# Kernel tuning notes

Measured on AMD Instinct MI355X. Metric: run time of the kernel, lower is better.

Reference implementation:

```python
import jax, jax.numpy as jnp
import numpy as np
from jax import lax

B, T, N, FIN = 1, 8, 50000, 3
E = 800000
HID, HEADS = 32, 2
NEG_SLOPE = 0.2  # PyG GATConv default negative_slope


def setup_inputs() -> dict:
    key = jax.random.key(0)
    ks = jax.random.split(key, 16)
    p = lambda k, shape: jax.random.normal(k, shape, dtype=jnp.float32) * 0.1
    return {
        "x_seq": jax.random.normal(ks[0], (B, T, N, FIN), dtype=jnp.float32),
        # GAT layer 1: lin weight [heads*hid, in], att vectors [heads, hid], bias [hid]
        "W1": p(ks[1], (HEADS * HID, FIN)),
        "a1_src": p(ks[2], (HEADS, HID)),
        "a1_dst": p(ks[3], (HEADS, HID)),
        "b1": p(ks[4], (HID,)),
        # GAT layer 2
        "W2": p(ks[5], (HEADS * HID, HID)),
        "a2_src": p(ks[6], (HEADS, HID)),
        "a2_dst": p(ks[7], (HEADS, HID)),
        "b2": p(ks[8], (HID,)),
        # GRU (single layer): torch layout [3*hid, hid] with gate order r,z,n
        "w_ih": p(ks[9], (3 * HID, HID)),
        "w_hh": p(ks[10], (3 * HID, HID)),
        "b_ih": p(ks[11], (3 * HID,)),
        "b_hh": p(ks[12], (3 * HID,)),
        # final Linear(hid, 1)
        "fc_w": p(ks[13], (1, HID)),
        "fc_b": p(ks[14], (1,)),
        "edge_index": jax.random.randint(ks[15], (2, E), 0, N, dtype=jnp.int64),
    }


def gat(x, src, dst, W, a_s, a_d, b):
    """PyG GATConv, heads=HEADS, concat=False (mean over heads). src/dst include self-loops."""
    n = x.shape[0]
    heads, hd = a_s.shape
    h = (x @ W.T).reshape(n, heads, hd)                      # [n, heads, hid]
    e = jax.nn.leaky_relu((h * a_s).sum(-1)[src] + (h * a_d).sum(-1)[dst], NEG_SLOPE)  # [E', heads]
    m = jax.ops.segment_max(e, dst, num_segments=n)          # per-destination max
    m = jnp.where(jnp.isfinite(m), m, jnp.zeros_like(m))
    ex = jnp.exp(e - m[dst])
    denom = jax.ops.segment_sum(ex, dst, num_segments=n)
    alpha = ex / (denom[dst] + 1e-16)                        # segment softmax
    out = jax.ops.segment_sum(h[src] * alpha[..., None], dst, num_segments=n)  # [n, heads, hid]
    return out.mean(axis=1) + b


def _forward(x_seq, W1, a1_src, a1_dst, b1, W2, a2_src, a2_dst, b2,
             w_ih, w_hh, b_ih, b_hh, fc_w, fc_b, edge_index):
    Bb, Tt, Nn, Fin = x_seq.shape
    n = Bb * Nn
    loops = jnp.arange(n, dtype=edge_index.dtype)            # add_self_loops=True
    src = jnp.concatenate([edge_index[0], loops])
    dst = jnp.concatenate([edge_index[1], loops])
    hid = b1.shape[0]

    def step(hstate, xt):                                    # one timestep: GAT x2 then GRU cell
        x = xt.reshape(n, Fin)
        g = jax.nn.relu(gat(x, src, dst, W1, a1_src, a1_dst, b1))
        g = jax.nn.relu(gat(g, src, dst, W2, a2_src, a2_dst, b2))
        gi = g @ w_ih.T + b_ih
        gh = hstate @ w_hh.T + b_hh
        i_r, i_z, i_n = jnp.split(gi, 3, axis=-1)
        h_r, h_z, h_n = jnp.split(gh, 3, axis=-1)
        r = jax.nn.sigmoid(i_r + h_r)
        z = jax.nn.sigmoid(i_z + h_z)
        cand = jnp.tanh(i_n + r * h_n)
        hnew = (1.0 - z) * cand + z * hstate
        return hnew, None

    h0 = jnp.zeros((n, hid), x_seq.dtype)
    h_final, _ = lax.scan(step, h0, jnp.moveaxis(x_seq, 1, 0))  # scan over T
    out = h_final @ fc_w.T + fc_b                            # [B*N, 1]
    return out.reshape(Bb, Nn)


def reference(x_seq, W1, a1_src, a1_dst, b1, W2, a2_src, a2_dst, b2,
              w_ih, w_hh, b_ih, b_hh, fc_w, fc_b, edge_index):
    return _forward(x_seq, W1, a1_src, a1_dst, b1, W2, a2_src, a2_dst, b2,
                    w_ih, w_hh, b_ih, b_hh, fc_w, fc_b, edge_index)
```

## Files before the change

kernel.cpp:

```cpp
#include <hip/hip_runtime.h>
#include <hip/hip_fp16.h>
#include <stdint.h>

#define T_STEPS 8
#define FIN 3
#define HID 32
#define NEG_SLOPE 0.2f
#define LOG2E 1.4426950408889634f

typedef __fp16 v4h __attribute__((ext_vector_type(4)));
typedef __fp16 v2h __attribute__((ext_vector_type(2)));
typedef float  v4f __attribute__((ext_vector_type(4)));

__device__ __forceinline__ float lrelu(float x) { return x > 0.f ? x : NEG_SLOPE * x; }
__device__ __forceinline__ float sigmoidf(float x) { return 1.f / (1.f + __expf(-x)); }

__device__ __forceinline__ float fdot2h(__half2 a, __half2 b, float c) {
#if __has_builtin(__builtin_amdgcn_fdot2)
    union { __half2 h; v2h v; } ua, ub;
    ua.h = a; ub.h = b;
    return __builtin_amdgcn_fdot2(ua.v, ub.v, c, false);
#else
    float2 fa = __half22float2(a), fb = __half22float2(b);
    return c + fa.x * fb.x + fa.y * fb.y;
#endif
}

__global__ void detect_kernel(const int* ei32, int nElems, int* flag) {
    __shared__ int any_nonzero;
    if (threadIdx.x == 0) any_nonzero = 0;
    __syncthreads();
    int idx = 1 + 2 * (int)threadIdx.x;
    if (idx < nElems && ei32[idx] != 0) any_nonzero = 1;
    __syncthreads();
    if (threadIdx.x == 0) *flag = (any_nonzero ? 0 : 1);
}

__device__ __forceinline__ int get_edge(const void* ei, int is64, long long idx) {
    if (is64) return (int)((const long long*)ei)[idx];
    return ((const int*)ei)[idx];
}

__global__ void init_kernel(int* cnt, int N) {
    int i = blockIdx.x * 256 + threadIdx.x;
    if (i < N) cnt[i] = 1;
}

__global__ void conv_count_kernel(const void* ei, const int* flag, int E, int N,
                                  int* src32, int* dst32, int* cnt) {
    int e = blockIdx.x * 256 + threadIdx.x;
    if (e >= E) return;
    int is64 = *flag;
    int s = get_edge(ei, is64, e);
    int d = get_edge(ei, is64, (long long)E + e);
    if ((unsigned)s >= (unsigned)N) s = 0;
    src32[e] = s;
    int dd = ((unsigned)d < (unsigned)N) ? d : 0x7fffffff;
    dst32[e] = dd;
    if (dd < N) atomicAdd(&cnt[dd], 1);
}

__global__ __launch_bounds__(256) void scan1_kernel(const int* cnt, int* rowptr, int* bsum, int n) {
    __shared__ int sm[256];
    int i = blockIdx.x * 256 + threadIdx.x;
    int v = (i < n) ? cnt[i] : 0;
    sm[threadIdx.x] = v;
    __syncthreads();
    for (int off = 1; off < 256; off <<= 1) {
        int t = (threadIdx.x >= off) ? sm[threadIdx.x - off] : 0;
        __syncthreads();
        sm[threadIdx.x] += t;
        __syncthreads();
    }
    if (i < n) rowptr[i + 1] = sm[threadIdx.x];
    if (threadIdx.x == 255) bsum[blockIdx.x] = sm[255];
}

__global__ __launch_bounds__(256) void scan2_kernel(int* bsum, int nb) {
    __shared__ int sm[256];
    int v = (threadIdx.x < nb) ? bsum[threadIdx.x] : 0;
    sm[threadIdx.x] = v;
    __syncthreads();
    for (int off = 1; off < 256; off <<= 1) {
        int t = (threadIdx.x >= off) ? sm[threadIdx.x - off] : 0;
        __syncthreads();
        sm[threadIdx.x] += t;
        __syncthreads();
    }
    if (threadIdx.x < nb) bsum[threadIdx.x] = sm[threadIdx.x];
}

__global__ __launch_bounds__(256) void scan3_kernel(int* rowptr, const int* bsum, int n) {
    int i = blockIdx.x * 256 + threadIdx.x;
    if (i < n && blockIdx.x > 0) rowptr[i + 1] += bsum[blockIdx.x - 1];
    if (i == 0) rowptr[0] = 0;
}

__global__ void selffill_kernel(const int* rowptr, int* csr, int* fill, int N) {
    int n = blockIdx.x * 256 + threadIdx.x;
    if (n >= N) return;
    int rp = rowptr[n];
    csr[rp] = n;
    fill[n] = rp + 1;
}

__global__ void scatter_kernel(const int* __restrict__ src32, const int* __restrict__ dst32,
                               int E, int lo, int hi, int* fill, int* csr) {
    int e = blockIdx.x * 256 + threadIdx.x;
    if (e >= E) return;
    int d = dst32[e];
    if (d < lo || d >= hi) return;
    int p = atomicAdd(&fill[d], 1);
    csr[p] = src32[e];
}

__global__ __launch_bounds__(64) void prep_u_kernel(
        const float* __restrict__ W2, const float* __restrict__ a2s,
        const float* __restrict__ a2d, float* __restrict__ u_s, float* __restrict__ u_d) {
    int l = threadIdx.x;
    int h = l >> 5, k = l & 31;
    float us = 0.f, ud = 0.f;
    for (int c = 0; c < 32; c++) {
        float w = W2[(h * 32 + c) * 32 + k];
        us += a2s[h * 32 + c] * w;
        ud += a2d[h * 32 + c] * w;
    }
    u_s[l] = us * LOG2E;
    u_d[l] = ud * LOG2E;
}

__global__ __launch_bounds__(256) void pack_kernel(
        const float* __restrict__ W2, __half2* __restrict__ w2h) {
    int idx = blockIdx.x * 256 + threadIdx.x;
    if (idx >= 1024) return;
    int kp = idx >> 6, r = idx & 63;
    float a = 0.5f * W2[r * 32 + 2 * kp];
    float b = 0.5f * W2[r * 32 + 2 * kp + 1];
    w2h[idx] = __floats2half2_rn(a, b);
}

__global__ __launch_bounds__(256) void packfrag_kernel(
        const float* __restrict__ w_ih, const float* __restrict__ w_hh,
        uint2* __restrict__ wfrag) {
    int idx = blockIdx.x * 256 + threadIdx.x;
    if (idx >= 1536) return;
    int q24 = idx >> 6, l = idx & 63;
    int c = l & 15, g = l >> 4;
    const float* W = (q24 < 12) ? w_ih : w_hh;
    int q = (q24 < 12) ? q24 : q24 - 12;
    int nt = q >> 1, kt = q & 1;
    float v[4];
#pragma unroll
    for (int b = 0; b < 4; b++) {
        int kk = kt * 16 + 4 * g + b;
        int nn = nt * 16 + c;
        v[b] = W[nn * 32 + kk];
    }
    __half2 lo = __floats2half2_rn(v[0], v[1]);
    __half2 hi = __floats2half2_rn(v[2], v[3]);
    uint2 u;
    u.x = *(unsigned*)&lo;
    u.y = *(unsigned*)&hi;
    wfrag[(8 + q24) * 64 + l] = u;
}

__global__ __launch_bounds__(256) void score1_all(
        const float* __restrict__ x_seq, const float* __restrict__ W1,
        const float* __restrict__ a1s, const float* __restrict__ a1d,
        float4* __restrict__ nrec4, float2* __restrict__ sd1, int N) {
    int t = blockIdx.x;
    int node = blockIdx.y * 256 + threadIdx.x;
    if (node >= N) return;
    const float* xp = x_seq + ((size_t)t * N + node) * FIN;
    float x0 = xp[0], x1 = xp[1], x2 = xp[2];
    float ps0 = 0.f, ps1 = 0.f, pd0 = 0.f, pd1 = 0.f;
    for (int c = 0; c < 32; c++) {
        float h0 = W1[c * 3] * x0 + W1[c * 3 + 1] * x1 + W1[c * 3 + 2] * x2;
        float h1 = W1[96 + c * 3] * x0 + W1[97 + c * 3] * x1 + W1[98 + c * 3] * x2;
        ps0 += h0 * a1s[c]; pd0 += h0 * a1d[c];
        ps1 += h1 * a1s[32 + c]; pd1 += h1 * a1d[32 + c];
    }
    ps0 *= LOG2E; ps1 *= LOG2E; pd0 *= LOG2E; pd1 *= LOG2E;
    unsigned u = (unsigned)__half_as_ushort(__float2half_rn(ps0)) |
                 ((unsigned)__half_as_ushort(__float2half_rn(ps1)) << 16);
    float4 r;
    r.x = x0; r.y = x1; r.z = x2; r.w = __uint_as_float(u);
    nrec4[(size_t)t * N + node] = r;
    sd1[(size_t)t * N + node] = make_float2(pd0, pd1);
}

__device__ __forceinline__ void unpack_scores(float wslot, float& s0, float& s1) {
    unsigned u = __float_as_uint(wslot);
    s0 = __half2float(__ushort_as_half((unsigned short)(u & 0xffffu)));
    s1 = __half2float(__ushort_as_half((unsigned short)(u >> 16)));
}

__global__ __launch_bounds__(64) void aggA_all(
        const int* __restrict__ rowptr, const int* __restrict__ csr,
        const float4* __restrict__ nrec4, const float2* __restrict__ sd1,
        const float* __restrict__ W1, const float* __restrict__ b1,
        const float* __restrict__ u_s, const float* __restrict__ u_d,
        __half2* __restrict__ g1h, float2* __restrict__ ssd2, float2* __restrict__ sd2, int N) {
    int t = blockIdx.x;
    int dst = blockIdx.y * 64 + threadIdx.x;
    if (dst >= N) return;
    const float4* nr = nrec4 + (size_t)t * N;
    int rs = rowptr[dst], re = rowptr[dst + 1];
    float2 sdv = sd1[(size_t)t * N + dst];
    float q0 = 0, qx0 = 0, qx1 = 0, qx2 = 0;
    float q1 = 0, qy0 = 0, qy1 = 0, qy2 = 0;
#define AGGA_EDGE(rr) { \
        float s0h, s1h; unpack_scores(rr.w, s0h, s1h); \
        float w0 = exp2f(lrelu(s0h + sdv.x)); \
        float w1 = exp2f(lrelu(s1h + sdv.y)); \
        q0 += w0; qx0 += w0 * rr.x; qx1 += w0 * rr.y; qx2 += w0 * rr.z; \
        q1 += w1; qy0 += w1 * rr.x; qy1 += w1 * rr.y; qy2 += w1 * rr.z; }
    int e = rs;
    for (; e + 4 <= re; e += 4) {
        int s0 = csr[e], s1 = csr[e + 1], s2 = csr[e + 2], s3 = csr[e + 3];
        float4 r0 = nr[s0], r1 = nr[s1], r2 = nr[s2], r3 = nr[s3];
        AGGA_EDGE(r0); AGGA_EDGE(r1); AGGA_EDGE(r2); AGGA_EDGE(r3);
    }
    for (; e < re; e++) {
        float4 r = nr[csr[e]];
        AGGA_EDGE(r);
    }
#undef AGGA_EDGE
    float inv0 = 1.f / (q0 + 1e-16f), inv1 = 1.f / (q1 + 1e-16f);
    float ax0 = qx0 * inv0, ax1 = qx1 * inv0, ax2 = qx2 * inv0;
    float ay0 = qy0 * inv1, ay1 = qy1 * inv1, ay2 = qy2 * inv1;
    float ps0 = 0, ps1 = 0, pd0 = 0, pd1 = 0;
    float4 out[4];
    __half2* ghp = (__half2*)out;
    float gprev = 0.f;
#pragma unroll
    for (int c = 0; c < 32; c++) {
        float v0 = W1[c * 3] * ax0 + W1[c * 3 + 1] * ax1 + W1[c * 3 + 2] * ax2;
        float v1 = W1[96 + c * 3] * ay0 + W1[97 + c * 3] * ay1 + W1[98 + c * 3] * ay2;
        float g = fmaxf(0.5f * (v0 + v1) + b1[c], 0.f);
        ps0 += g * u_s[c];      ps1 += g * u_s[32 + c];
        pd0 += g * u_d[c];      pd1 += g * u_d[32 + c];
        if (c & 1) ghp[c >> 1] = __floats2half2_rn(gprev, g);
        else gprev = g;
    }
    float4* gdst = (float4*)(g1h + (size_t)t * N * 16 + (size_t)dst * 16);
    gdst[0] = out[0]; gdst[1] = out[1]; gdst[2] = out[2]; gdst[3] = out[3];
    ssd2[(size_t)t * N + dst] = make_float2(ps0, ps1);
    sd2[(size_t)t * N + dst]  = make_float2(pd0, pd1);
}

__global__ __launch_bounds__(256) void aggBg2_all(
        const int* __restrict__ rowptr, const int* __restrict__ csr,
        const __half2* __restrict__ g1h,
        const float2* __restrict__ ssd2, const float2* __restrict__ sd2,
        const __half2* __restrict__ w2h, const float* __restrict__ b2,
        __half2* __restrict__ g2H, int N) {
    __shared__ __half2 a_lds[64 * 33];
    int t = blockIdx.x;
    int tid = threadIdx.x;
    int node0 = blockIdx.y * 64;
    int dl = tid >> 2;
    int q = tid & 3;
    int dst = node0 + dl;
    if (dst < N) {
        const __half2* gbase = g1h + (size_t)t * N * 16 + q * 4;
        const float2* ss = ssd2 + (size_t)t * N;
        int rs = rowptr[dst], re = rowptr[dst + 1];
        float2 sdv = sd2[(size_t)t * N + dst];
        float a0[8] = {0, 0, 0, 0, 0, 0, 0, 0};
        float a1[8] = {0, 0, 0, 0, 0, 0, 0, 0};
        float den0 = 0.f, den1 = 0.f;
#define AGGB_EDGE(sc, gv) { \
        float w0 = exp2f(lrelu(sc.x + sdv.x)); \
        float w1 = exp2f(lrelu(sc.y + sdv.y)); \
        den0 += w0; den1 += w1; \
        __half2 w0h = __float2half2_rn(w0); \
        __half2 w1h = __float2half2_rn(w1); \
        const __half2* p = (const __half2*)&(gv); \
        h0[0] = __hfma2(w0h, p[0], h0[0]); h0[1] = __hfma2(w0h, p[1], h0[1]); \
        h0[2] = __hfma2(w0h, p[2], h0[2]); h0[3] = __hfma2(w0h, p[3], h0[3]); \
        h1[0] = __hfma2(w1h, p[0], h1[0]); h1[1] = __hfma2(w1h, p[1], h1[1]); \
        h1[2] = __hfma2(w1h, p[2], h1[2]); h1[3] = __hfma2(w1h, p[3], h1[3]); }
        int e = rs;
        while (e < re) {
            int lim = min(re, e + 16);
            __half2 h0[4], h1[4];
#pragma unroll
            for (int j = 0; j < 4; j++) {
                h0[j] = __floats2half2_rn(0.f, 0.f);
                h1[j] = __floats2half2_rn(0.f, 0.f);
            }
            for (; e + 4 <= lim; e += 4) {
                int s0 = csr[e], s1 = csr[e + 1], s2 = csr[e + 2], s3 = csr[e + 3];
                float2 c0 = ss[s0], c1 = ss[s1], c2 = ss[s2], c3 = ss[s3];
                float4 g0 = *(const float4*)(gbase + (size_t)s0 * 16);
                float4 g1 = *(const float4*)(gbase + (size_t)s1 * 16);
                float4 g2 = *(const float4*)(gbase + (size_t)s2 * 16);
                float4 g3 = *(const float4*)(gbase + (size_t)s3 * 16);
                AGGB_EDGE(c0, g0); AGGB_EDGE(c1, g1); AGGB_EDGE(c2, g2); AGGB_EDGE(c3, g3);
            }
            for (; e < lim; e++) {
                int s = csr[e];
                float2 c = ss[s];
                float4 g = *(const float4*)(gbase + (size_t)s * 16);
                AGGB_EDGE(c, g);
            }
#pragma unroll
            for (int j = 0; j < 4; j++) {
                float2 v0 = __half22float2(h0[j]);
                float2 v1 = __half22float2(h1[j]);
                a0[2 * j] += v0.x; a0[2 * j + 1] += v0.y;
                a1[2 * j] += v1.x; a1[2 * j + 1] += v1.y;
            }
        }
#undef AGGB_EDGE
        float i0 = 1.f / (den0 + 1e-16f), i1 = 1.f / (den1 + 1e-16f);
#pragma unroll
        for (int j = 0; j < 4; j++) {
            a_lds[dl * 33 + q * 4 + j]      = __floats2half2_rn(a0[2 * j] * i0, a0[2 * j + 1] * i0);
            a_lds[dl * 33 + 16 + q * 4 + j] = __floats2half2_rn(a1[2 * j] * i1, a1[2 * j + 1] * i1);
        }
    }
    __syncthreads();
    int nl = tid & 63;
    int cg8 = __builtin_amdgcn_readfirstlane((tid >> 6) * 8);
    int node = node0 + nl;
    if (node >= N) return;
    float acc[8] = {0, 0, 0, 0, 0, 0, 0, 0};
    for (int kp = 0; kp < 16; kp++) {
        __half2 A0 = a_lds[nl * 33 + kp];
        __half2 A1 = a_lds[nl * 33 + 16 + kp];
        const __half2* w0p = w2h + kp * 64 + cg8;
        const __half2* w1p = w2h + kp * 64 + 32 + cg8;
#pragma unroll
        for (int j = 0; j < 8; j++) {
            acc[j] = fdot2h(A0, w0p[j], acc[j]);
            acc[j] = fdot2h(A1, w1p[j], acc[j]);
        }
    }
    __half2 o[4];
#pragma unroll
    for (int j = 0; j < 4; j++) {
        float ga = fmaxf(acc[2 * j] + b2[cg8 + 2 * j], 0.f);
        float gb = fmaxf(acc[2 * j + 1] + b2[cg8 + 2 * j + 1], 0.f);
        o[j] = __floats2half2_rn(ga, gb);
    }
    *(float4*)(g2H + ((size_t)t * N + node) * 16 + (cg8 >> 1)) = *(float4*)o;
}

__global__ __launch_bounds__(64) void gru_mfma(
        const __half2* __restrict__ g2H, const uint2* __restrict__ wfrag,
        const float* __restrict__ b_ih, const float* __restrict__ b_hh,
        const float* __restrict__ fc_w, const float* __restrict__ fc_b,
        float* __restrict__ out, int N) {
    __shared__ __align__(16) __half h_lds[16 * 36];
    int l = threadIdx.x;
    int c = l & 15;
    int g4 = l >> 4;
    int node0 = blockIdx.x * 16;
    union FU { uint2 u; v4h h; };
    v4h Bih[6][2], Bhh[6][2];
#pragma unroll
    for (int nt = 0; nt < 6; nt++)
#pragma unroll
        for (int kt = 0; kt < 2; kt++) {
            FU f; f.u = wfrag[(8 + nt * 2 + kt) * 64 + l]; Bih[nt][kt] = f.h;
            f.u = wfrag[(20 + nt * 2 + kt) * 64 + l]; Bhh[nt][kt] = f.h;
        }
    float bir0 = b_ih[c], bir1 = b_ih[c + 16];
    float biz0 = b_ih[32 + c], biz1 = b_ih[48 + c];
    float bin0 = b_ih[64 + c], bin1 = b_ih[80 + c];
    float bhr0 = b_hh[c], bhr1 = b_hh[c + 16];
    float bhz0 = b_hh[32 + c], bhz1 = b_hh[48 + c];
    float bhn0 = b_hh[64 + c], bhn1 = b_hh[80 + c];
    float fcw0 = fc_w[c], fcw1 = fc_w[c + 16];
    v4f hold0 = {0.f, 0.f, 0.f, 0.f};
    v4f hold1 = {0.f, 0.f, 0.f, 0.f};
    const __half2* rowb = g2H + (size_t)(node0 + c) * 16;
    for (int t = 0; t < T_STEPS; t++) {
        const __half2* rb = rowb + (size_t)t * N * 16;
        v4f Di[6], Dh[6];
#pragma unroll
        for (int nt = 0; nt < 6; nt++) { Di[nt] = {0.f, 0.f, 0.f, 0.f}; Dh[nt] = {0.f, 0.f, 0.f, 0.f}; }
#pragma unroll
        for (int kt = 0; kt < 2; kt++) {
            FU Ag; Ag.u = *(const uint2*)(rb + 2 * g4 + 8 * kt);
#pragma unroll
            for (int nt = 0; nt < 6; nt++)
                Di[nt] = __builtin_amdgcn_mfma_f32_16x16x16f16(Ag.h, Bih[nt][kt], Di[nt], 0, 0, 0);
        }
        if (t > 0) {
#pragma unroll
            for (int kt = 0; kt < 2; kt++) {
                FU Ah; Ah.u = *(const uint2*)&h_lds[c * 36 + 4 * g4 + 16 * kt];
#pragma unroll
                for (int nt = 0; nt < 6; nt++)
                    Dh[nt] = __builtin_amdgcn_mfma_f32_16x16x16f16(Ah.h, Bhh[nt][kt], Dh[nt], 0, 0, 0);
            }
        }
        v4f hn0, hn1;
#pragma unroll
        for (int i = 0; i < 4; i++) {
            {
                float rr = sigmoidf((Di[0][i] + bir0) + (Dh[0][i] + bhr0));
                float zz = sigmoidf((Di[2][i] + biz0) + (Dh[2][i] + bhz0));
                float cand = tanhf((Di[4][i] + bin0) + rr * (Dh[4][i] + bhn0));
                hn0[i] = (1.f - zz) * cand + zz * hold0[i];
            }
            {
                float rr = sigmoidf((Di[1][i] + bir1) + (Dh[1][i] + bhr1));
                float zz = sigmoidf((Di[3][i] + biz1) + (Dh[3][i] + bhz1));
                float cand = tanhf((Di[5][i] + bin1) + rr * (Dh[5][i] + bhn1));
                hn1[i] = (1.f - zz) * cand + zz * hold1[i];
            }
        }
        hold0 = hn0; hold1 = hn1;
        if (t < T_STEPS - 1) {
            __syncthreads();
#pragma unroll
            for (int i = 0; i < 4; i++) {
                int nrow = 4 * g4 + i;
                h_lds[nrow * 36 + c]      = __float2half_rn(hn0[i]);
                h_lds[nrow * 36 + c + 16] = __float2half_rn(hn1[i]);
            }
            __syncthreads();
        }
    }
#pragma unroll
    for (int i = 0; i < 4; i++) {
        float p = fcw0 * hold0[i] + fcw1 * hold1[i];
        p += __shfl_xor(p, 1, 64);
        p += __shfl_xor(p, 2, 64);
        p += __shfl_xor(p, 4, 64);
        p += __shfl_xor(p, 8, 64);
        if (c == 0) out[node0 + 4 * g4 + i] = p + fc_b[0];
    }
}

extern "C" void kernel_launch(void* const* d_in, const int* in_sizes, int n_in,
                              void* d_out, int out_size, void* d_ws, size_t ws_size,
                              hipStream_t stream) {
    const float* x_seq = (const float*)d_in[0];
    const float* W1  = (const float*)d_in[1];
    const float* a1s = (const float*)d_in[2];
    const float* a1d = (const float*)d_in[3];
    const float* b1  = (const float*)d_in[4];
    const float* W2  = (const float*)d_in[5];
    const float* a2s = (const float*)d_in[6];
    const float* a2d = (const float*)d_in[7];
    const float* b2  = (const float*)d_in[8];
    const float* w_ih = (const float*)d_in[9];
    const float* w_hh = (const float*)d_in[10];
    const float* b_ih = (const float*)d_in[11];
    const float* b_hh = (const float*)d_in[12];
    const float* fc_w = (const float*)d_in[13];
    const float* fc_b = (const float*)d_in[14];
    const void*  ei   = d_in[15];

    const int N = in_sizes[0] / (T_STEPS * FIN);
    const int E = in_sizes[15] / 2;
    const int NE = E + N;
    const int NB = (N + 255) / 256;
    const int NB64 = (N + 63) / 64;
    const int NB16 = (N + 15) / 16;
    const int EB = (E + 255) / 256;

    char* ws = (char*)d_ws;
    size_t off = 0;
    auto alloc = [&](size_t bytes) -> void* {
        void* p = ws + off;
        off += (bytes + 255) & ~(size_t)255;
        return p;
    };
    int*     flag   = (int*)alloc(4);
    int*     rowptr = (int*)alloc((size_t)(N + 1) * 4);
    int*     cnt    = (int*)alloc((size_t)N * 4);
    int*     bsum   = (int*)alloc(256 * 4);
    int*     csr    = (int*)alloc((size_t)NE * 4);
    int*     src32  = (int*)alloc((size_t)E * 4);
    int*     dst32  = (int*)alloc((size_t)E * 4);
    float4*  nrec4  = (float4*)alloc((size_t)T_STEPS * N * 16);
    float2*  sd1    = (float2*)alloc((size_t)T_STEPS * N * 8);
    float2*  ssd2   = (float2*)alloc((size_t)T_STEPS * N * 8);
    float2*  sd2    = (float2*)alloc((size_t)T_STEPS * N * 8);
    __half2* g1h    = (__half2*)alloc((size_t)T_STEPS * N * 16 * 4);
    __half2* g2H    = (__half2*)alloc((size_t)T_STEPS * N * 16 * 4);
    float*   u_s    = (float*)alloc(64 * 4);
    float*   u_d    = (float*)alloc(64 * 4);
    __half2* w2h    = (__half2*)alloc(1024 * 4);
    uint2*   wfrag  = (uint2*)alloc(32 * 64 * 8);
    if (off > ws_size) return;

    detect_kernel<<<1, 128, 0, stream>>>((const int*)ei, in_sizes[15], flag);
    init_kernel<<<NB, 256, 0, stream>>>(cnt, N);
    conv_count_kernel<<<EB, 256, 0, stream>>>(ei, flag, E, N, src32, dst32, cnt);
    scan1_kernel<<<NB, 256, 0, stream>>>(cnt, rowptr, bsum, N);
    scan2_kernel<<<1, 256, 0, stream>>>(bsum, NB);
    scan3_kernel<<<NB, 256, 0, stream>>>(rowptr, bsum, N);
    selffill_kernel<<<NB, 256, 0, stream>>>(rowptr, csr, cnt, N);
    {
        const int NPASS = 2;
        int per = (N + NPASS - 1) / NPASS;
        for (int p = 0; p < NPASS; p++) {
            int lo = p * per;
            int hi = min(lo + per, N);
            scatter_kernel<<<EB, 256, 0, stream>>>(src32, dst32, E, lo, hi, cnt, csr);
        }
    }
    prep_u_kernel<<<1, 64, 0, stream>>>(W2, a2s, a2d, u_s, u_d);
    pack_kernel<<<4, 256, 0, stream>>>(W2, w2h);
    packfrag_kernel<<<6, 256, 0, stream>>>(w_ih, w_hh, wfrag);

    score1_all<<<dim3(T_STEPS, NB), 256, 0, stream>>>(x_seq, W1, a1s, a1d, nrec4, sd1, N);
    aggA_all<<<dim3(T_STEPS, NB64), 64, 0, stream>>>(rowptr, csr, nrec4, sd1, W1, b1,
                                                     u_s, u_d, g1h, ssd2, sd2, N);
    aggBg2_all<<<dim3(T_STEPS, NB64), 256, 0, stream>>>(rowptr, csr, g1h, ssd2, sd2,
                                                        w2h, b2, g2H, N);
    gru_mfma<<<NB16, 64, 0, stream>>>(g2H, wfrag, b_ih, b_hh,
                                      fc_w, fc_b, (float*)d_out, N);
}
```

Before: 289.8 us.

## Process one destination node per thread in layer-2 aggregation and projection

The layer-2 aggregation kernel drops the four-threads-per-node split with an LDS staging buffer and a block barrier. Each thread now owns one destination node. It gathers full 64-byte source rows, accumulates all 32 channels for both heads, and does the full 32x32 projection in registers before writing its output row. This removes the LDS round trip, the synchronization and the redundant per-node score/rowptr loads. In exchange it sharply raises register pressure (64 float accumulators plus 32 half2 partials), lowers gather parallelism per node and increases divergence across nodes of different degree.

```diff
diff --git a/kernel.cpp b/kernel.cpp
--- a/kernel.cpp
+++ b/kernel.cpp
@@ -255,97 +255,91 @@
         const float2* __restrict__ ssd2, const float2* __restrict__ sd2,
         const __half2* __restrict__ w2h, const float* __restrict__ b2,
         __half2* __restrict__ g2H, int N) {
-    __shared__ __half2 a_lds[64 * 33];
     int t = blockIdx.x;
-    int tid = threadIdx.x;
-    int node0 = blockIdx.y * 64;
-    int dl = tid >> 2;
-    int q = tid & 3;
-    int dst = node0 + dl;
-    if (dst < N) {
-        const __half2* gbase = g1h + (size_t)t * N * 16 + q * 4;
-        const float2* ss = ssd2 + (size_t)t * N;
-        int rs = rowptr[dst], re = rowptr[dst + 1];
-        float2 sdv = sd2[(size_t)t * N + dst];
-        float a0[8] = {0, 0, 0, 0, 0, 0, 0, 0};
-        float a1[8] = {0, 0, 0, 0, 0, 0, 0, 0};
-        float den0 = 0.f, den1 = 0.f;
-#define AGGB_EDGE(sc, gv) { \
+    int dst = blockIdx.y * 256 + threadIdx.x;
+    if (dst >= N) return;
+    const __half2* gt = g1h + (size_t)t * N * 16;
+    const float2* ss = ssd2 + (size_t)t * N;
+    int rs = rowptr[dst], re = rowptr[dst + 1];
+    float2 sdv = sd2[(size_t)t * N + dst];
+    float den0 = 0.f, den1 = 0.f;
+    float a0f[32], a1f[32];
+#pragma unroll
+    for (int j = 0; j < 32; j++) { a0f[j] = 0.f; a1f[j] = 0.f; }
+    union Row { float4 f[4]; __half2 h[16]; };
+#define AGGB_EDGE(sc, rr) { \
         float w0 = exp2f(lrelu(sc.x + sdv.x)); \
         float w1 = exp2f(lrelu(sc.y + sdv.y)); \
         den0 += w0; den1 += w1; \
         __half2 w0h = __float2half2_rn(w0); \
         __half2 w1h = __float2half2_rn(w1); \
-        const __half2* p = (const __half2*)&(gv); \
-        h0[0] = __hfma2(w0h, p[0], h0[0]); h0[1] = __hfma2(w0h, p[1], h0[1]); \
-        h0[2] = __hfma2(w0h, p[2], h0[2]); h0[3] = __hfma2(w0h, p[3], h0[3]); \
-        h1[0] = __hfma2(w1h, p[0], h1[0]); h1[1] = __hfma2(w1h, p[1], h1[1]); \
-        h1[2] = __hfma2(w1h, p[2], h1[2]); h1[3] = __hfma2(w1h, p[3], h1[3]); }
-        int e = rs;
-        while (e < re) {
-            int lim = min(re, e + 16);
-            __half2 h0[4], h1[4];
-#pragma unroll
-            for (int j = 0; j < 4; j++) {
-                h0[j] = __floats2half2_rn(0.f, 0.f);
-                h1[j] = __floats2half2_rn(0.f, 0.f);
-            }
-            for (; e + 4 <= lim; e += 4) {
-                int s0 = csr[e], s1 = csr[e + 1], s2 = csr[e + 2], s3 = csr[e + 3];
-                float2 c0 = ss[s0], c1 = ss[s1], c2 = ss[s2], c3 = ss[s3];
-                float4 g0 = *(const float4*)(gbase + (size_t)s0 * 16);
-                float4 g1 = *(const float4*)(gbase + (size_t)s1 * 16);
-                float4 g2 = *(const float4*)(gbase + (size_t)s2 * 16);
-                float4 g3 = *(const float4*)(gbase + (size_t)s3 * 16);
-                AGGB_EDGE(c0, g0); AGGB_EDGE(c1, g1); AGGB_EDGE(c2, g2); AGGB_EDGE(c3, g3);
-            }
-            for (; e < lim; e++) {
-                int s = csr[e];
-                float2 c = ss[s];
-                float4 g = *(const float4*)(gbase + (size_t)s * 16);
-                AGGB_EDGE(c, g);
-            }
-#pragma unroll
-            for (int j = 0; j < 4; j++) {
-                float2 v0 = __half22float2(h0[j]);
-                float2 v1 = __half22float2(h1[j]);
-                a0[2 * j] += v0.x; a0[2 * j + 1] += v0.y;
-                a1[2 * j] += v1.x; a1[2 * j + 1] += v1.y;
-            }
-        }
+        _Pragma("unroll") \
+        for (int j = 0; j < 16; j++) { \
+            p0[j] = __hfma2(w0h, rr.h[j], p0[j]); \
+            p1[j] = __hfma2(w1h, rr.h[j], p1[j]); \
+        } }
+    int e = rs;
+    while (e < re) {
+        int lim = min(re, e + 16);
+        __half2 p0[16], p1[16];
+        __half2 z = __floats2half2_rn(0.f, 0.f);
+#pragma unroll
+        for (int j = 0; j < 16; j++) { p0[j] = z; p1[j] = z; }
+        for (; e + 2 <= lim; e += 2) {
+            int s0 = csr[e], s1 = csr[e + 1];
+            float2 c0 = ss[s0], c1 = ss[s1];
+            const float4* r0p = (const float4*)(gt + (size_t)s0 * 16);
+            const float4* r1p = (const float4*)(gt + (size_t)s1 * 16);
+            Row r0, r1;
+            r0.f[0] = r0p[0]; r0.f[1] = r0p[1]; r0.f[2] = r0p[2]; r0.f[3] = r0p[3];
+            r1.f[0] = r1p[0]; r1.f[1] = r1p[1]; r1.f[2] = r1p[2]; r1.f[3] = r1p[3];
+            AGGB_EDGE(c0, r0);
+            AGGB_EDGE(c1, r1);
+        }
+        for (; e < lim; e++) {
+            int s = csr[e];
+            float2 c = ss[s];
+            const float4* rp = (const float4*)(gt + (size_t)s * 16);
+            Row r;
+            r.f[0] = rp[0]; r.f[1] = rp[1]; r.f[2] = rp[2]; r.f[3] = rp[3];
+            AGGB_EDGE(c, r);
+        }
+#pragma unroll
+        for (int j = 0; j < 16; j++) {
+            float2 v0 = __half22float2(p0[j]);
+            float2 v1 = __half22float2(p1[j]);
+            a0f[2 * j] += v0.x; a0f[2 * j + 1] += v0.y;
+            a1f[2 * j] += v1.x; a1f[2 * j + 1] += v1.y;
+        }
+    }
 #undef AGGB_EDGE
-        float i0 = 1.f / (den0 + 1e-16f), i1 = 1.f / (den1 + 1e-16f);
-#pragma unroll
-        for (int j = 0; j < 4; j++) {
-            a_lds[dl * 33 + q * 4 + j]      = __floats2half2_rn(a0[2 * j] * i0, a0[2 * j + 1] * i0);
-            a_lds[dl * 33 + 16 + q * 4 + j] = __floats2half2_rn(a1[2 * j] * i1, a1[2 * j + 1] * i1);
-        }
-    }
-    __syncthreads();
-    int nl = tid & 63;
-    int cg8 = __builtin_amdgcn_readfirstlane((tid >> 6) * 8);
-    int node = node0 + nl;
-    if (node >= N) return;
-    float acc[8] = {0, 0, 0, 0, 0, 0, 0, 0};
-    for (int kp = 0; kp < 16; kp++) {
-        __half2 A0 = a_lds[nl * 33 + kp];
-        __half2 A1 = a_lds[nl * 33 + 16 + kp];
-        const __half2* w0p = w2h + kp * 64 + cg8;
-        const __half2* w1p = w2h + kp * 64 + 32 + cg8;
-#pragma unroll
-        for (int j = 0; j < 8; j++) {
-            acc[j] = fdot2h(A0, w0p[j], acc[j]);
-            acc[j] = fdot2h(A1, w1p[j], acc[j]);
-        }
-    }
-    __half2 o[4];
-#pragma unroll
-    for (int j = 0; j < 4; j++) {
-        float ga = fmaxf(acc[2 * j] + b2[cg8 + 2 * j], 0.f);
-        float gb = fmaxf(acc[2 * j + 1] + b2[cg8 + 2 * j + 1], 0.f);
-        o[j] = __floats2half2_rn(ga, gb);
-    }
-    *(float4*)(g2H + ((size_t)t * N + node) * 16 + (cg8 >> 1)) = *(float4*)o;
+    float i0 = 1.f / (den0 + 1e-16f), i1 = 1.f / (den1 + 1e-16f);
+    __half2 an0[16], an1[16];
+#pragma unroll
+    for (int j = 0; j < 16; j++) {
+        an0[j] = __floats2half2_rn(a0f[2 * j] * i0, a0f[2 * j + 1] * i0);
+        an1[j] = __floats2half2_rn(a1f[2 * j] * i1, a1f[2 * j + 1] * i1);
+    }
+    __half2 og[16];
+#pragma unroll
+    for (int cp = 0; cp < 16; cp++) {
+        float accA = 0.f, accB = 0.f;
+#pragma unroll
+        for (int kp = 0; kp < 16; kp++) {
+            accA = fdot2h(an0[kp], w2h[kp * 64 + 2 * cp], accA);
+            accA = fdot2h(an1[kp], w2h[kp * 64 + 32 + 2 * cp], accA);
+            accB = fdot2h(an0[kp], w2h[kp * 64 + 2 * cp + 1], accB);
+            accB = fdot2h(an1[kp], w2h[kp * 64 + 32 + 2 * cp + 1], accB);
+        }
+        float ga = fmaxf(accA + b2[2 * cp], 0.f);
+        float gb = fmaxf(accB + b2[2 * cp + 1], 0.f);
+        og[cp] = __floats2half2_rn(ga, gb);
+    }
+    float4* o = (float4*)(g2H + ((size_t)t * N + dst) * 16);
+    o[0] = ((float4*)og)[0];
+    o[1] = ((float4*)og)[1];
+    o[2] = ((float4*)og)[2];
+    o[3] = ((float4*)og)[3];
 }
 
 __global__ __launch_bounds__(64) void gru_mfma(
@@ -514,8 +508,8 @@
     score1_all<<<dim3(T_STEPS, NB), 256, 0, stream>>>(x_seq, W1, a1s, a1d, nrec4, sd1, N);
     aggA_all<<<dim3(T_STEPS, NB64), 64, 0, stream>>>(rowptr, csr, nrec4, sd1, W1, b1,
                                                      u_s, u_d, g1h, ssd2, sd2, N);
-    aggBg2_all<<<dim3(T_STEPS, NB64), 256, 0, stream>>>(rowptr, csr, g1h, ssd2, sd2,
-                                                        w2h, b2, g2H, N);
+    aggBg2_all<<<dim3(T_STEPS, NB), 256, 0, stream>>>(rowptr, csr, g1h, ssd2, sd2,
+                                                      w2h, b2, g2H, N);
     gru_mfma<<<NB16, 64, 0, stream>>>(g2H, wfrag, b_ih, b_hh,
                                       fc_w, fc_b, (float*)d_out, N);
 }
```

Result: slower. 321.5 us (+11.0%).
